# Kernel tuning notes

Measured on AMD Instinct MI355X. Metric: run time of the kernel, lower is better.

Reference implementation:

```python
import jax, jax.numpy as jnp
import numpy as np

N = 100_000   # nodes
E = 3_200_000 # edges (avg degree 32)
H = 128       # hidden units
G = 64        # graphs in batch
EPS = 1e-5    # BatchNorm eps


def setup_inputs() -> dict:
    key = jax.random.key(0)
    ks = jax.random.split(key, 32)
    s = 0.05
    inp = {
        "x": jax.random.normal(ks[0], (N, 1), dtype=jnp.float32),
        "edge_index": jax.random.randint(ks[1], (2, E), 0, N, dtype=jnp.int64 if jax.config.jax_enable_x64 else jnp.int32),
        "batch": jnp.sort(jax.random.randint(ks[2], (N,), 0, G, dtype=jnp.int64 if jax.config.jax_enable_x64 else jnp.int32)),
    }
    dims = [(1, H), (H, H), (H, H)]
    k = 3
    for li, (cin, cout) in enumerate(dims, start=1):
        inp[f"W_rel{li}"] = jax.random.normal(ks[k], (cout, cin), dtype=jnp.float32) * s; k += 1
        inp[f"b_rel{li}"] = jax.random.normal(ks[k], (cout,), dtype=jnp.float32) * s; k += 1
        inp[f"W_root{li}"] = jax.random.normal(ks[k], (cout, cin), dtype=jnp.float32) * s; k += 1
        inp[f"gamma{li}"] = jnp.ones((cout,), dtype=jnp.float32)
        inp[f"beta{li}"] = jnp.zeros((cout,), dtype=jnp.float32)
        inp[f"mean{li}"] = jax.random.normal(ks[k], (cout,), dtype=jnp.float32) * s; k += 1
        inp[f"var{li}"] = jax.random.uniform(ks[k], (cout,), dtype=jnp.float32, minval=0.5, maxval=1.5); k += 1
    inp["W_out"] = jax.random.normal(ks[k], (1, H), dtype=jnp.float32) * s; k += 1
    inp["b_out"] = jax.random.normal(ks[k], (1,), dtype=jnp.float32) * s
    return inp


def _graph_conv(x, src, dst, W_rel, b_rel, W_root):
    # PyG GraphConv (aggr='add'): out_i = W_rel @ sum_{j->i} x_j + b_rel + W_root @ x_i
    agg = jax.ops.segment_sum(x[src], dst, num_segments=N)  # [N, Cin]
    return agg @ W_rel.T + b_rel + x @ W_root.T


def _bn_eval(x, gamma, beta, mean, var):
    return (x - mean) * jax.lax.rsqrt(var + EPS) * gamma + beta


def reference(x, edge_index, batch,
              W_rel1, b_rel1, W_root1, gamma1, beta1, mean1, var1,
              W_rel2, b_rel2, W_root2, gamma2, beta2, mean2, var2,
              W_rel3, b_rel3, W_root3, gamma3, beta3, mean3, var3,
              W_out, b_out):
    src, dst = edge_index[0], edge_index[1]
    h = _graph_conv(x, src, dst, W_rel1, b_rel1, W_root1)
    h = jax.nn.relu(_bn_eval(h, gamma1, beta1, mean1, var1))  # dropout p=0 / eval -> identity
    h = _graph_conv(h, src, dst, W_rel2, b_rel2, W_root2)
    h = jax.nn.relu(_bn_eval(h, gamma2, beta2, mean2, var2))
    h = _graph_conv(h, src, dst, W_rel3, b_rel3, W_root3)
    h = _bn_eval(h, gamma3, beta3, mean3, var3)
    # global mean pool over graphs
    sums = jax.ops.segment_sum(h, batch, num_segments=G)                       # [G, H]
    cnts = jax.ops.segment_sum(jnp.ones((N, 1), h.dtype), batch, num_segments=G)
    pooled = sums / jnp.maximum(cnts, 1.0)
    return pooled @ W_out.T + b_out  # [G, 1]
```

## Files before the change

### kernel.cpp

```cpp
#include <hip/hip_runtime.h>

typedef unsigned int uint;
typedef unsigned short ushort;
typedef unsigned char uchar;

#define EPS 1e-5f
#define BSH 8
#define NBMAX 512
#define BCAP 10240
#define SCAT_E 8192

typedef __attribute__((ext_vector_type(8))) short short8;
typedef __attribute__((ext_vector_type(16))) float f32x16;
typedef __attribute__((ext_vector_type(2))) float float2v;
typedef __attribute__((ext_vector_type(2))) _Float16 half2v;
typedef __attribute__((ext_vector_type(8))) _Float16 f16x8;

static __device__ __forceinline__ ushort f2h(float f) {
    return __builtin_bit_cast(ushort, (_Float16)f);
}
static __device__ __forceinline__ half2v u2h(uint u) {
    return __builtin_bit_cast(half2v, u);
}

__global__ __launch_bounds__(256) void hist2d_kernel(const int* __restrict__ dst,
                                                     int* __restrict__ cnt2d, int E, int NB) {
    __shared__ int lh[NBMAX];
    const int tid = threadIdx.x;
    for (int t = tid; t < NB; t += 256) lh[t] = 0;
    __syncthreads();
    const int base = blockIdx.x * SCAT_E, end = min(base + SCAT_E, E);
    for (int i = base + tid; i < end; i += 256) atomicAdd(&lh[dst[i] >> BSH], 1);
    __syncthreads();
    int* row = cnt2d + (size_t)blockIdx.x * NB;
    for (int t = tid; t < NB; t += 256) row[t] = lh[t];
}

__global__ __launch_bounds__(256) void scan2d_kernel(int* __restrict__ cnt2d,
                                                     int* __restrict__ bcnt, int NB, int NBLK) {
    const int b = blockIdx.x * 4 + (threadIdx.x >> 6);
    if (b >= NB) return;
    const int lane = threadIdx.x & 63;
    int carry = 0;
    for (int c0 = 0; c0 < NBLK; c0 += 64) {
        int idx = c0 + lane;
        int v = (idx < NBLK) ? cnt2d[(size_t)idx * NB + b] : 0;
        int inc = v;
#pragma unroll
        for (int d = 1; d < 64; d <<= 1) { int u = __shfl_up(inc, d); if (lane >= d) inc += u; }
        if (idx < NBLK) cnt2d[(size_t)idx * NB + b] = inc - v + carry;
        carry += __shfl(inc, 63);
    }
    if (lane == 0) bcnt[b] = carry;
}

__global__ void scan_gcur_kernel(const int* __restrict__ bcnt, int* __restrict__ gcur, int nb) {
    __shared__ int wsum[4];
    const int t = threadIdx.x;
    int e[4], s = 0;
#pragma unroll
    for (int k = 0; k < 4; ++k) {
        int idx = t * 4 + k;
        e[k] = (idx < nb) ? bcnt[idx] : 0;
        s += e[k];
    }
    int lane = t & 63, w = t >> 6;
    int v = s;
#pragma unroll
    for (int d = 1; d < 64; d <<= 1) { int u = __shfl_up(v, d); if (lane >= d) v += u; }
    if (lane == 63) wsum[w] = v;
    __syncthreads();
    int off = 0;
    for (int k = 0; k < w; ++k) off += wsum[k];
    int run = off + v - s;
#pragma unroll
    for (int k = 0; k < 4; ++k) {
        int idx = t * 4 + k;
        if (idx < nb) gcur[idx] = run;
        run += e[k];
    }
    if (t == 0) gcur[nb] = wsum[0] + wsum[1] + wsum[2] + wsum[3];
}

__global__ __launch_bounds__(256) void bucket_scatter_kernel(const int* __restrict__ src,
                                                             const int* __restrict__ dst,
                                                             const int* __restrict__ gcur,
                                                             const int* __restrict__ cnt2d,
                                                             uint* __restrict__ stage,
                                                             int E, int NB) {
    __shared__ uint sedge[SCAT_E];
    __shared__ ushort sbkt[SCAT_E];
    __shared__ int lh[NBMAX];
    __shared__ int lofs[NBMAX + 1];
    __shared__ int lbase[NBMAX];
    __shared__ int wsum[4];
    const int tid = threadIdx.x;
    const int base = blockIdx.x * SCAT_E;
    const int len = min(base + SCAT_E, E) - base;
    const int* myrow = cnt2d + (size_t)blockIdx.x * NB;

    for (int t = tid; t < NB; t += 256) lh[t] = 0;
    __syncthreads();
    for (int i = tid; i < len; i += 256) atomicAdd(&lh[dst[base + i] >> BSH], 1);
    __syncthreads();
    const int i0 = tid * 2, i1 = tid * 2 + 1;
    int e0 = (i0 < NB) ? lh[i0] : 0;
    int e1 = (i1 < NB) ? lh[i1] : 0;
    int s = e0 + e1;
    int lane = tid & 63, w = tid >> 6;
    int v = s;
#pragma unroll
    for (int d = 1; d < 64; d <<= 1) { int u = __shfl_up(v, d); if (lane >= d) v += u; }
    if (lane == 63) wsum[w] = v;
    __syncthreads();
    int off = 0;
    for (int k = 0; k < w; ++k) off += wsum[k];
    int run = off + v - s;
    if (i0 <= NB) lofs[i0] = run;
    if (i0 < NB) lbase[i0] = gcur[i0] + myrow[i0];
    run += e0;
    if (i1 <= NB) lofs[i1] = run;
    if (i1 < NB) lbase[i1] = gcur[i1] + myrow[i1];
    __syncthreads();
    for (int t = tid; t < NB; t += 256) lh[t] = 0;
    __syncthreads();
    for (int i = tid; i < len; i += 256) {
        int d = dst[base + i];
        int b = d >> BSH;
        int r = atomicAdd(&lh[b], 1);
        int pos = lofs[b] + r;
        sedge[pos] = (uint)src[base + i] | ((uint)(d & 255) << 17);
        sbkt[pos] = (ushort)b;
    }
    __syncthreads();
    for (int i = tid; i < len; i += 256) {
        int b = sbkt[i];
        stage[lbase[b] + (i - lofs[b])] = sedge[i];
    }
}

__global__ __launch_bounds__(256) void bucket_final_kernel(const uint* __restrict__ stage,
                                                           const int* __restrict__ gcur,
                                                           int* __restrict__ rowptr,
                                                           int* __restrict__ eidx, int n) {
    __shared__ uint sbuf[BCAP];
    __shared__ int cnt[256];
    __shared__ int wsum[4];
    const int b = blockIdx.x, tid = threadIdx.x;
    const int r0 = gcur[b];
    const int r1 = gcur[b + 1];
    const int len = r1 - r0;
    const bool inl = (len <= BCAP);
    cnt[tid] = 0;
    if (inl) for (int i = tid; i < len; i += 256) sbuf[i] = stage[r0 + i];
    __syncthreads();
    for (int i = tid; i < len; i += 256) {
        uint v = inl ? sbuf[i] : stage[r0 + i];
        atomicAdd(&cnt[v >> 17], 1);
    }
    __syncthreads();
    int orig = cnt[tid], v = orig;
    int lane = tid & 63, w = tid >> 6;
#pragma unroll
    for (int d2 = 1; d2 < 64; d2 <<= 1) { int u = __shfl_up(v, d2); if (lane >= d2) v += u; }
    if (lane == 63) wsum[w] = v;
    __syncthreads();
    int off = 0;
    for (int k = 0; k < w; ++k) off += wsum[k];
    const int excl = r0 + off + v - orig;
    const int d = (b << BSH) + tid;
    if (d <= n) rowptr[d] = excl;
    __syncthreads();
    cnt[tid] = excl;
    __syncthreads();
    for (int i = tid; i < len; i += 256) {
        uint pv = inl ? sbuf[i] : stage[r0 + i];
        int slot = atomicAdd(&cnt[pv >> 17], 1);
        eidx[slot] = (int)(pv & 0x1FFFFu);
    }
}

__global__ __launch_bounds__(256) void layer1_fused_kernel(
    const float* __restrict__ x, const int* __restrict__ rowptr, const int* __restrict__ eidx,
    const float* __restrict__ Wrel, const float* __restrict__ brel,
    const float* __restrict__ Wroot, const float* __restrict__ gamma,
    const float* __restrict__ beta, const float* __restrict__ mean,
    const float* __restrict__ var, ushort* __restrict__ h1, uchar* __restrict__ h8, int n) {
    __shared__ float A[128], B[128], C[128];
    const int tid = threadIdx.x;
    if (tid < 128) {
        float sc = gamma[tid] * rsqrtf(var[tid] + EPS);
        A[tid] = Wrel[tid] * sc;
        B[tid] = Wroot[tid] * sc;
        C[tid] = beta[tid] + (brel[tid] - mean[tid]) * sc;
    }
    __syncthreads();
    const int g16 = tid >> 4;
    const int l16 = tid & 15;
    const int node = blockIdx.x * 16 + g16;
    if (node >= n) return;
    const int e0 = rowptr[node], e1 = rowptr[node + 1];
    float acc = 0.f;
    for (int e = e0 + l16; e < e1; e += 16) acc += x[eidx[e]];
#pragma unroll
    for (int d = 1; d < 16; d <<= 1) acc += __shfl_xor(acc, d);
    const float xi = x[node];
    float vv[8];
    uint4 o;
    ushort* op = (ushort*)&o;
#pragma unroll
    for (int j = 0; j < 8; ++j) {
        int c = l16 * 8 + j;
        vv[j] = fmaxf(acc * A[c] + xi * B[c] + C[c], 0.f);
        op[j] = f2h(vv[j]);
    }
    *((uint4*)(h1 + (size_t)node * 128) + l16) = o;
    uint p0 = 0, p1 = 0;
    p0 = __builtin_amdgcn_cvt_pk_fp8_f32(vv[0], vv[1], 0, 0);
    p0 = __builtin_amdgcn_cvt_pk_fp8_f32(vv[2], vv[3], p0, 1);
    p1 = __builtin_amdgcn_cvt_pk_fp8_f32(vv[4], vv[5], 0, 0);
    p1 = __builtin_amdgcn_cvt_pk_fp8_f32(vv[6], vv[7], p1, 1);
    uint2 o8; o8.x = p0; o8.y = p1;
    ((uint2*)(h8 + (size_t)node * 128))[l16] = o8;
}

__global__ __launch_bounds__(256) void gather_fp8_kernel(const uchar* __restrict__ h8,
                                                         const int* __restrict__ rowptr,
                                                         const int* __restrict__ eidx,
                                                         ushort* __restrict__ agg, int n) {
    const int node = blockIdx.x * 4 + (threadIdx.x >> 6);
    if (node >= n) return;
    const int lane = threadIdx.x & 63;
    const int g = lane >> 4;
    const int c8 = lane & 15;
    const uint2* hq = (const uint2*)h8;
    const int e0 = rowptr[node];
    const int len = rowptr[node + 1] - e0;

    float2v a0 = {0.f, 0.f}, a1 = {0.f, 0.f}, a2 = {0.f, 0.f}, a3 = {0.f, 0.f};

#define ACC8(u)                                                        \
    do {                                                               \
        a0 += __builtin_amdgcn_cvt_pk_f32_fp8((int)(u).x, 0);          \
        a1 += __builtin_amdgcn_cvt_pk_f32_fp8((int)(u).x, 1);          \
        a2 += __builtin_amdgcn_cvt_pk_f32_fp8((int)(u).y, 0);          \
        a3 += __builtin_amdgcn_cvt_pk_f32_fp8((int)(u).y, 1);          \
    } while (0)

    for (int base = 0; base < len; base += 64) {
        const int cnt = min(len - base, 64);
        int msrc = (lane < cnt) ? eidx[e0 + base + lane] : 0;
        const int kfull = cnt >> 2;
        int k = 0;
        for (; k + 8 <= kfull; k += 8) {
            uint2 u[8];
#pragma unroll
            for (int s = 0; s < 8; ++s) {
                int src = __shfl(msrc, (k + s) * 4 + g);
                u[s] = hq[(size_t)src * 16 + c8];
            }
#pragma unroll
            for (int s = 0; s < 8; ++s) ACC8(u[s]);
        }
        for (; k < kfull; ++k) {
            int src = __shfl(msrc, k * 4 + g);
            uint2 u = hq[(size_t)src * 16 + c8];
            ACC8(u);
        }
        const int rem = cnt & 3;
        if (rem) {
            int idx = (kfull << 2) + g;
            int src = __shfl(msrc, idx);
            if (g < rem) {
                uint2 u = hq[(size_t)src * 16 + c8];
                ACC8(u);
            }
        }
    }
#undef ACC8

#pragma unroll
    for (int d = 16; d <= 32; d <<= 1) {
        a0[0] += __shfl_xor(a0[0], d); a0[1] += __shfl_xor(a0[1], d);
        a1[0] += __shfl_xor(a1[0], d); a1[1] += __shfl_xor(a1[1], d);
        a2[0] += __shfl_xor(a2[0], d); a2[1] += __shfl_xor(a2[1], d);
        a3[0] += __shfl_xor(a3[0], d); a3[1] += __shfl_xor(a3[1], d);
    }
    if (g == 0) {
        uint4 o;
        ushort* op = (ushort*)&o;
        op[0] = f2h(a0[0]); op[1] = f2h(a0[1]);
        op[2] = f2h(a1[0]); op[3] = f2h(a1[1]);
        op[4] = f2h(a2[0]); op[5] = f2h(a2[1]);
        op[6] = f2h(a3[0]); op[7] = f2h(a3[1]);
        ((uint4*)agg)[(size_t)node * 16 + c8] = o;
    }
}

__global__ void wf_prep_kernel(const float* __restrict__ W0, const float* __restrict__ W1,
                               const float* __restrict__ W2, const float* __restrict__ W3,
                               ushort* __restrict__ WF2, ushort* __restrict__ WF3) {
    int i = blockIdx.x * 256 + threadIdx.x;
    const float* Ws[4] = {W0, W1, W2, W3};
    int mat = i >> 14;
    int m = i & 16383;
    int j = m & 7, lane = (m >> 3) & 63, ct = (m >> 9) & 3, kt = (m >> 11) & 7;
    int row = ct * 32 + (lane & 31);
    int col = kt * 16 + ((lane >> 5) * 8) + j;
    float v = Ws[mat][row * 128 + col];
    ushort* dstp = (mat < 2) ? WF2 : WF3;
    dstp[(mat & 1) * 16384 + m] = f2h(v);
}

template <int RELU, int WRITE8>
__global__ __launch_bounds__(256) void conv_mfma_kernel(
    const short* __restrict__ agg, const short* __restrict__ hin,
    const short* __restrict__ WF,
    const float* __restrict__ brel, const float* __restrict__ gamma,
    const float* __restrict__ beta, const float* __restrict__ mean,
    const float* __restrict__ var,
    ushort* __restrict__ hout, uchar* __restrict__ h8out, int n) {
    const int lane = threadIdx.x & 63;
    const int wt = blockIdx.x * 4 + (threadIdx.x >> 6);
    const int node0 = wt * 32;
    if (node0 >= n) return;
    const int rowA = node0 + (lane & 31);
    const int arow = (rowA < n) ? rowA : (n - 1);
    const int koff = (lane >> 5) * 8;

    f32x16 acc[4];
#pragma unroll
    for (int c = 0; c < 4; ++c) acc[c] = (f32x16)(0.0f);

#pragma unroll
    for (int half = 0; half < 2; ++half) {
        const short* A = (half ? hin : agg) + (size_t)arow * 128 + koff;
        const short* B0 = WF + half * 16384 + lane * 8;
#pragma unroll
        for (int kt = 0; kt < 8; ++kt) {
            f16x8 a = __builtin_bit_cast(f16x8, *(const short8*)(A + kt * 16));
            const short* Bp = B0 + kt * 2048;
#pragma unroll
            for (int ct = 0; ct < 4; ++ct) {
                f16x8 b = __builtin_bit_cast(f16x8, *(const short8*)(Bp + ct * 512));
                acc[ct] = __builtin_amdgcn_mfma_f32_32x32x16_f16(a, b, acc[ct], 0, 0, 0);
            }
        }
    }

#pragma unroll
    for (int ct = 0; ct < 4; ++ct) {
        int c = ct * 32 + (lane & 31);
        float s = gamma[c] * rsqrtf(var[c] + EPS);
        float t = beta[c] - mean[c] * s + brel[c] * s;
#pragma unroll
        for (int r = 0; r < 16; ++r) {
            int row = (r & 3) + 8 * (r >> 2) + 4 * (lane >> 5);
            int node = node0 + row;
            if (node < n) {
                float v = acc[ct][r] * s + t;
                if (RELU) v = fmaxf(v, 0.f);
                hout[(size_t)node * 128 + c] = f2h(v);
                if (WRITE8) {
                    uint p = __builtin_amdgcn_cvt_pk_fp8_f32(v, v, 0, 0);
                    h8out[(size_t)node * 128 + c] = (uchar)p;
                }
            }
        }
    }
}

__global__ __launch_bounds__(256) void pool_kernel(const ushort* __restrict__ h,
                                                   const int* __restrict__ batch,
                                                   const float* __restrict__ Wout,
                                                   float* __restrict__ gscal,
                                                   int* __restrict__ gcnt, int n) {
    const int wv = blockIdx.x * 4 + (threadIdx.x >> 6);
    const int lane = threadIdx.x & 63;
    const int base = wv * 64;
    if (base >= n) return;
    const int end = min(base + 64, n);
    const uint* hu = (const uint*)h;
    const float w0 = Wout[lane * 2], w1 = Wout[lane * 2 + 1];
    float s = 0.f;
    int cur = batch[base], cl = 0;

    auto accum = [&](uint u) {
        half2v hv = u2h(u);
        s += (float)hv[0] * w0 + (float)hv[1] * w1;
        cl++;
    };
    auto flush = [&](int g) {
        float r = s;
#pragma unroll
        for (int d = 1; d < 64; d <<= 1) r += __shfl_xor(r, d);
        if (lane == 0) { atomicAdd(&gscal[g], r); atomicAdd(&gcnt[g], cl); }
        s = 0.f; cl = 0;
    };

    int i = base;
    for (; i + 4 <= end; i += 4) {
        int b3 = batch[i + 3];
        uint u0 = hu[(size_t)i * 64 + lane];
        uint u1 = hu[(size_t)(i + 1) * 64 + lane];
        uint u2 = hu[(size_t)(i + 2) * 64 + lane];
        uint u3 = hu[(size_t)(i + 3) * 64 + lane];
        if (b3 == cur) {
            accum(u0); accum(u1); accum(u2); accum(u3);
        } else {
            int bb[4] = {batch[i], batch[i + 1], batch[i + 2], b3};
            uint uu[4] = {u0, u1, u2, u3};
            for (int k = 0; k < 4; ++k) {
                if (bb[k] != cur) { flush(cur); cur = bb[k]; }
                accum(uu[k]);
            }
        }
    }
    for (; i < end; ++i) {
        int g = batch[i];
        if (g != cur) { flush(cur); cur = g; }
        accum(hu[(size_t)i * 64 + lane]);
    }
    flush(cur);
}

__global__ void out_kernel(const float* __restrict__ gscal, const int* __restrict__ gcnt,
                           const float* __restrict__ bout, float* __restrict__ out, int G) {
    int g = threadIdx.x;
    if (g < G) out[g] = gscal[g] / fmaxf((float)gcnt[g], 1.0f) + bout[0];
}

extern "C" void kernel_launch(void* const* d_in, const int* in_sizes, int n_in,
                              void* d_out, int out_size, void* d_ws, size_t ws_size,
                              hipStream_t stream) {
    const int N = in_sizes[0];
    const int E = in_sizes[1] / 2;
    const int G = 64;

    const float* x     = (const float*)d_in[0];
    const int*   ei    = (const int*)d_in[1];
    const int*   batch = (const int*)d_in[2];
    const int*   src   = ei;
    const int*   dst   = ei + E;

    const float* Wrel1 = (const float*)d_in[3];
    const float* brel1 = (const float*)d_in[4];
    const float* Wroot1= (const float*)d_in[5];
    const float* g1    = (const float*)d_in[6];
    const float* be1   = (const float*)d_in[7];
    const float* m1    = (const float*)d_in[8];
    const float* v1    = (const float*)d_in[9];
    const float* Wrel2 = (const float*)d_in[10];
    const float* brel2 = (const float*)d_in[11];
    const float* Wroot2= (const float*)d_in[12];
    const float* g2    = (const float*)d_in[13];
    const float* be2   = (const float*)d_in[14];
    const float* m2    = (const float*)d_in[15];
    const float* v2    = (const float*)d_in[16];
    const float* Wrel3 = (const float*)d_in[17];
    const float* brel3 = (const float*)d_in[18];
    const float* Wroot3= (const float*)d_in[19];
    const float* g3    = (const float*)d_in[20];
    const float* be3   = (const float*)d_in[21];
    const float* m3    = (const float*)d_in[22];
    const float* v3    = (const float*)d_in[23];
    const float* Wout  = (const float*)d_in[24];
    const float* bout  = (const float*)d_in[25];

    float* out = (float*)d_out;

    const int NB   = (N >> BSH) + 1;
    const int NBLK = (E + SCAT_E - 1) / SCAT_E;

    char* w = (char*)d_ws;
    auto alloc = [&](size_t bytes) { char* p = w; w += (bytes + 511) & ~(size_t)511; return p; };
    int*    rowptr = (int*)alloc((size_t)(N + 1) * 4);
    int*    bcnt   = (int*)alloc(NBMAX * 4);
    int*    gcur   = (int*)alloc((NBMAX + 1) * 4);
    int*    cnt2d  = (int*)alloc((size_t)NBLK * NB * 4);
    uint*   stage  = (uint*)alloc((size_t)E * 4);
    int*    eidx   = (int*)alloc((size_t)E * 4);
    ushort* hA     = (ushort*)alloc((size_t)N * 128 * 2);
    ushort* hB     = (ushort*)alloc((size_t)N * 128 * 2);
    ushort* aggb   = (ushort*)alloc((size_t)N * 128 * 2);
    uchar*  h8     = (uchar*)alloc((size_t)N * 128);
    ushort* WF2    = (ushort*)alloc(32768 * 2);
    ushort* WF3    = (ushort*)alloc(32768 * 2);
    float*  gscal  = (float*)alloc((size_t)G * 4);
    int*    gcnt   = (int*)alloc((size_t)G * 4);

    hipMemsetAsync(gscal, 0, (size_t)G * 4, stream);
    hipMemsetAsync(gcnt, 0, (size_t)G * 4, stream);

    hist2d_kernel<<<NBLK, 256, 0, stream>>>(dst, cnt2d, E, NB);
    scan2d_kernel<<<(NB + 3) / 4, 256, 0, stream>>>(cnt2d, bcnt, NB, NBLK);
    scan_gcur_kernel<<<1, 256, 0, stream>>>(bcnt, gcur, NB);
    bucket_scatter_kernel<<<NBLK, 256, 0, stream>>>(src, dst, gcur, cnt2d, stage, E, NB);
    bucket_final_kernel<<<NB, 256, 0, stream>>>(stage, gcur, rowptr, eidx, N);

    wf_prep_kernel<<<256, 256, 0, stream>>>(Wrel2, Wroot2, Wrel3, Wroot3, WF2, WF3);

    layer1_fused_kernel<<<(N + 15) / 16, 256, 0, stream>>>(x, rowptr, eidx, Wrel1, brel1,
                                                           Wroot1, g1, be1, m1, v1, hA, h8, N);

    const int nwt     = (N + 31) / 32;
    const int convBlk = (nwt + 3) / 4;
    const int gBlk    = (N + 3) / 4;

    gather_fp8_kernel<<<gBlk, 256, 0, stream>>>(h8, rowptr, eidx, aggb, N);
    conv_mfma_kernel<1, 1><<<convBlk, 256, 0, stream>>>((const short*)aggb, (const short*)hA,
                                                        (const short*)WF2, brel2, g2, be2, m2, v2,
                                                        hB, h8, N);

    gather_fp8_kernel<<<gBlk, 256, 0, stream>>>(h8, rowptr, eidx, aggb, N);
    conv_mfma_kernel<0, 0><<<convBlk, 256, 0, stream>>>((const short*)aggb, (const short*)hB,
                                                        (const short*)WF3, brel3, g3, be3, m3, v3,
                                                        hA, (uchar*)nullptr, N);

    pool_kernel<<<(N + 255) / 256, 256, 0, stream>>>(hA, batch, Wout, gscal, gcnt, N);
    out_kernel<<<1, 64, 0, stream>>>(gscal, gcnt, bout, out, G);
}
```

Measured before the change: 300.6 us.

## Fuse fp8 gather, MFMA conv and mean-pool into a single per-layer kernel

Merges the neighbor gather into the MFMA GraphConv kernel. Each block gathers 32 nodes' aggregated features into swizzled LDS and then multiplies them directly, so the fp16 agg buffer is never written to or read from global memory. The last layer also folds the output projection and per-graph pooling into the epilogue using LDS atomics, which removes the hA write and the separate pool kernel. Ping-pong fp8 buffers replace the single h8 buffer so a layer's write does not race its own gather reads. The trade-offs are fewer blocks with serialized per-wave gathers (8 nodes per wave), one output column tile per wave, and LDS atomics in the pool epilogue.

```diff
diff --git a/kernel.cpp b/kernel.cpp
--- a/kernel.cpp
+++ b/kernel.cpp
@@ -224,79 +224,6 @@
     ((uint2*)(h8 + (size_t)node * 128))[l16] = o8;
 }
 
-__global__ __launch_bounds__(256) void gather_fp8_kernel(const uchar* __restrict__ h8,
-                                                         const int* __restrict__ rowptr,
-                                                         const int* __restrict__ eidx,
-                                                         ushort* __restrict__ agg, int n) {
-    const int node = blockIdx.x * 4 + (threadIdx.x >> 6);
-    if (node >= n) return;
-    const int lane = threadIdx.x & 63;
-    const int g = lane >> 4;
-    const int c8 = lane & 15;
-    const uint2* hq = (const uint2*)h8;
-    const int e0 = rowptr[node];
-    const int len = rowptr[node + 1] - e0;
-
-    float2v a0 = {0.f, 0.f}, a1 = {0.f, 0.f}, a2 = {0.f, 0.f}, a3 = {0.f, 0.f};
-
-#define ACC8(u)                                                        \
-    do {                                                               \
-        a0 += __builtin_amdgcn_cvt_pk_f32_fp8((int)(u).x, 0);          \
-        a1 += __builtin_amdgcn_cvt_pk_f32_fp8((int)(u).x, 1);          \
-        a2 += __builtin_amdgcn_cvt_pk_f32_fp8((int)(u).y, 0);          \
-        a3 += __builtin_amdgcn_cvt_pk_f32_fp8((int)(u).y, 1);          \
-    } while (0)
-
-    for (int base = 0; base < len; base += 64) {
-        const int cnt = min(len - base, 64);
-        int msrc = (lane < cnt) ? eidx[e0 + base + lane] : 0;
-        const int kfull = cnt >> 2;
-        int k = 0;
-        for (; k + 8 <= kfull; k += 8) {
-            uint2 u[8];
-#pragma unroll
-            for (int s = 0; s < 8; ++s) {
-                int src = __shfl(msrc, (k + s) * 4 + g);
-                u[s] = hq[(size_t)src * 16 + c8];
-            }
-#pragma unroll
-            for (int s = 0; s < 8; ++s) ACC8(u[s]);
-        }
-        for (; k < kfull; ++k) {
-            int src = __shfl(msrc, k * 4 + g);
-            uint2 u = hq[(size_t)src * 16 + c8];
-            ACC8(u);
-        }
-        const int rem = cnt & 3;
-        if (rem) {
-            int idx = (kfull << 2) + g;
-            int src = __shfl(msrc, idx);
-            if (g < rem) {
-                uint2 u = hq[(size_t)src * 16 + c8];
-                ACC8(u);
-            }
-        }
-    }
-#undef ACC8
-
-#pragma unroll
-    for (int d = 16; d <= 32; d <<= 1) {
-        a0[0] += __shfl_xor(a0[0], d); a0[1] += __shfl_xor(a0[1], d);
-        a1[0] += __shfl_xor(a1[0], d); a1[1] += __shfl_xor(a1[1], d);
-        a2[0] += __shfl_xor(a2[0], d); a2[1] += __shfl_xor(a2[1], d);
-        a3[0] += __shfl_xor(a3[0], d); a3[1] += __shfl_xor(a3[1], d);
-    }
-    if (g == 0) {
-        uint4 o;
-        ushort* op = (ushort*)&o;
-        op[0] = f2h(a0[0]); op[1] = f2h(a0[1]);
-        op[2] = f2h(a1[0]); op[3] = f2h(a1[1]);
-        op[4] = f2h(a2[0]); op[5] = f2h(a2[1]);
-        op[6] = f2h(a3[0]); op[7] = f2h(a3[1]);
-        ((uint4*)agg)[(size_t)node * 16 + c8] = o;
-    }
-}
-
 __global__ void wf_prep_kernel(const float* __restrict__ W0, const float* __restrict__ W1,
                                const float* __restrict__ W2, const float* __restrict__ W3,
                                ushort* __restrict__ WF2, ushort* __restrict__ WF3) {
@@ -312,53 +239,125 @@
     dstp[(mat & 1) * 16384 + m] = f2h(v);
 }
 
-template <int RELU, int WRITE8>
-__global__ __launch_bounds__(256) void conv_mfma_kernel(
-    const short* __restrict__ agg, const short* __restrict__ hin,
-    const short* __restrict__ WF,
+template <int RELU, int WRITE8, int POOL>
+__global__ __launch_bounds__(256) void gc_kernel(
+    const uchar* __restrict__ h8in, const int* __restrict__ rowptr, const int* __restrict__ eidx,
+    const short* __restrict__ hin, const short* __restrict__ WF,
     const float* __restrict__ brel, const float* __restrict__ gamma,
     const float* __restrict__ beta, const float* __restrict__ mean,
     const float* __restrict__ var,
-    ushort* __restrict__ hout, uchar* __restrict__ h8out, int n) {
-    const int lane = threadIdx.x & 63;
-    const int wt = blockIdx.x * 4 + (threadIdx.x >> 6);
-    const int node0 = wt * 32;
-    if (node0 >= n) return;
-    const int rowA = node0 + (lane & 31);
-    const int arow = (rowA < n) ? rowA : (n - 1);
+    ushort* __restrict__ hout, uchar* __restrict__ h8out,
+    const int* __restrict__ batch, const float* __restrict__ Wout,
+    float* __restrict__ gscal, int* __restrict__ gcnt, int n) {
+    __shared__ uint4 aggL[32][16];
+    __shared__ float pg[64];
+    __shared__ int pc[64];
+    const int tid = threadIdx.x;
+    if (POOL && tid < 64) { pg[tid] = 0.f; pc[tid] = 0; }
+    const int w = tid >> 6, lane = tid & 63, g = lane >> 4, c8 = lane & 15;
+    const uint2* hq = (const uint2*)h8in;
+    const int T = blockIdx.x * 32;
+
+    for (int nd = 0; nd < 8; ++nd) {
+        const int rr = w * 8 + nd;
+        const int node = T + rr;
+        if (node >= n) break;
+        const int e0 = rowptr[node];
+        const int len = rowptr[node + 1] - e0;
+        float2v a0 = {0.f, 0.f}, a1 = {0.f, 0.f}, a2 = {0.f, 0.f}, a3 = {0.f, 0.f};
+
+#define ACC8(u)                                                        \
+    do {                                                               \
+        a0 += __builtin_amdgcn_cvt_pk_f32_fp8((int)(u).x, 0);          \
+        a1 += __builtin_amdgcn_cvt_pk_f32_fp8((int)(u).x, 1);          \
+        a2 += __builtin_amdgcn_cvt_pk_f32_fp8((int)(u).y, 0);          \
+        a3 += __builtin_amdgcn_cvt_pk_f32_fp8((int)(u).y, 1);          \
+    } while (0)
+
+        for (int base = 0; base < len; base += 64) {
+            const int cnt = min(len - base, 64);
+            int msrc = (lane < cnt) ? eidx[e0 + base + lane] : 0;
+            const int kfull = cnt >> 2;
+            int k = 0;
+            for (; k + 8 <= kfull; k += 8) {
+                uint2 u[8];
+#pragma unroll
+                for (int s = 0; s < 8; ++s) {
+                    int src = __shfl(msrc, (k + s) * 4 + g);
+                    u[s] = hq[(size_t)src * 16 + c8];
+                }
+#pragma unroll
+                for (int s = 0; s < 8; ++s) ACC8(u[s]);
+            }
+            for (; k < kfull; ++k) {
+                int src = __shfl(msrc, k * 4 + g);
+                uint2 u = hq[(size_t)src * 16 + c8];
+                ACC8(u);
+            }
+            const int rem = cnt & 3;
+            if (rem) {
+                int idx = (kfull << 2) + g;
+                int src = __shfl(msrc, idx);
+                if (g < rem) {
+                    uint2 u = hq[(size_t)src * 16 + c8];
+                    ACC8(u);
+                }
+            }
+        }
+#undef ACC8
+#pragma unroll
+        for (int d = 16; d <= 32; d <<= 1) {
+            a0[0] += __shfl_xor(a0[0], d); a0[1] += __shfl_xor(a0[1], d);
+            a1[0] += __shfl_xor(a1[0], d); a1[1] += __shfl_xor(a1[1], d);
+            a2[0] += __shfl_xor(a2[0], d); a2[1] += __shfl_xor(a2[1], d);
+            a3[0] += __shfl_xor(a3[0], d); a3[1] += __shfl_xor(a3[1], d);
+        }
+        if (g == 0) {
+            uint4 o;
+            ushort* op = (ushort*)&o;
+            op[0] = f2h(a0[0]); op[1] = f2h(a0[1]);
+            op[2] = f2h(a1[0]); op[3] = f2h(a1[1]);
+            op[4] = f2h(a2[0]); op[5] = f2h(a2[1]);
+            op[6] = f2h(a3[0]); op[7] = f2h(a3[1]);
+            aggL[rr][c8 ^ (rr & 7)] = o;
+        }
+    }
+    __syncthreads();
+
+    const int ct = w;
+    const int r32 = lane & 31;
     const int koff = (lane >> 5) * 8;
-
-    f32x16 acc[4];
-#pragma unroll
-    for (int c = 0; c < 4; ++c) acc[c] = (f32x16)(0.0f);
-
-#pragma unroll
-    for (int half = 0; half < 2; ++half) {
-        const short* A = (half ? hin : agg) + (size_t)arow * 128 + koff;
-        const short* B0 = WF + half * 16384 + lane * 8;
+    const int arow = (T + r32 < n) ? (T + r32) : (n - 1);
+    f32x16 acc = (f32x16)(0.0f);
+    {
+        const short* B0 = WF + ct * 512 + lane * 8;
 #pragma unroll
         for (int kt = 0; kt < 8; ++kt) {
-            f16x8 a = __builtin_bit_cast(f16x8, *(const short8*)(A + kt * 16));
-            const short* Bp = B0 + kt * 2048;
-#pragma unroll
-            for (int ct = 0; ct < 4; ++ct) {
-                f16x8 b = __builtin_bit_cast(f16x8, *(const short8*)(Bp + ct * 512));
-                acc[ct] = __builtin_amdgcn_mfma_f32_32x32x16_f16(a, b, acc[ct], 0, 0, 0);
-            }
-        }
-    }
-
-#pragma unroll
-    for (int ct = 0; ct < 4; ++ct) {
-        int c = ct * 32 + (lane & 31);
-        float s = gamma[c] * rsqrtf(var[c] + EPS);
-        float t = beta[c] - mean[c] * s + brel[c] * s;
+            int ch = 2 * kt + (koff >> 3);
+            uint4 av = aggL[r32][ch ^ (r32 & 7)];
+            f16x8 a = __builtin_bit_cast(f16x8, av);
+            f16x8 b = __builtin_bit_cast(f16x8, *(const short8*)(B0 + kt * 2048));
+            acc = __builtin_amdgcn_mfma_f32_32x32x16_f16(a, b, acc, 0, 0, 0);
+        }
+        const short* A1 = hin + (size_t)arow * 128 + koff;
+        const short* B1 = WF + 16384 + ct * 512 + lane * 8;
+#pragma unroll
+        for (int kt = 0; kt < 8; ++kt) {
+            f16x8 a = __builtin_bit_cast(f16x8, *(const short8*)(A1 + kt * 16));
+            f16x8 b = __builtin_bit_cast(f16x8, *(const short8*)(B1 + kt * 2048));
+            acc = __builtin_amdgcn_mfma_f32_32x32x16_f16(a, b, acc, 0, 0, 0);
+        }
+    }
+    const int c = ct * 32 + r32;
+    float s = gamma[c] * rsqrtf(var[c] + EPS);
+    float t = beta[c] - mean[c] * s + brel[c] * s;
+    if (!POOL) {
 #pragma unroll
         for (int r = 0; r < 16; ++r) {
             int row = (r & 3) + 8 * (r >> 2) + 4 * (lane >> 5);
-            int node = node0 + row;
+            int node = T + row;
             if (node < n) {
-                float v = acc[ct][r] * s + t;
+                float v = acc[r] * s + t;
                 if (RELU) v = fmaxf(v, 0.f);
                 hout[(size_t)node * 128 + c] = f2h(v);
                 if (WRITE8) {
@@ -367,61 +366,27 @@
                 }
             }
         }
-    }
-}
-
-__global__ __launch_bounds__(256) void pool_kernel(const ushort* __restrict__ h,
-                                                   const int* __restrict__ batch,
-                                                   const float* __restrict__ Wout,
-                                                   float* __restrict__ gscal,
-                                                   int* __restrict__ gcnt, int n) {
-    const int wv = blockIdx.x * 4 + (threadIdx.x >> 6);
-    const int lane = threadIdx.x & 63;
-    const int base = wv * 64;
-    if (base >= n) return;
-    const int end = min(base + 64, n);
-    const uint* hu = (const uint*)h;
-    const float w0 = Wout[lane * 2], w1 = Wout[lane * 2 + 1];
-    float s = 0.f;
-    int cur = batch[base], cl = 0;
-
-    auto accum = [&](uint u) {
-        half2v hv = u2h(u);
-        s += (float)hv[0] * w0 + (float)hv[1] * w1;
-        cl++;
-    };
-    auto flush = [&](int g) {
-        float r = s;
-#pragma unroll
-        for (int d = 1; d < 64; d <<= 1) r += __shfl_xor(r, d);
-        if (lane == 0) { atomicAdd(&gscal[g], r); atomicAdd(&gcnt[g], cl); }
-        s = 0.f; cl = 0;
-    };
-
-    int i = base;
-    for (; i + 4 <= end; i += 4) {
-        int b3 = batch[i + 3];
-        uint u0 = hu[(size_t)i * 64 + lane];
-        uint u1 = hu[(size_t)(i + 1) * 64 + lane];
-        uint u2 = hu[(size_t)(i + 2) * 64 + lane];
-        uint u3 = hu[(size_t)(i + 3) * 64 + lane];
-        if (b3 == cur) {
-            accum(u0); accum(u1); accum(u2); accum(u3);
-        } else {
-            int bb[4] = {batch[i], batch[i + 1], batch[i + 2], b3};
-            uint uu[4] = {u0, u1, u2, u3};
-            for (int k = 0; k < 4; ++k) {
-                if (bb[k] != cur) { flush(cur); cur = bb[k]; }
-                accum(uu[k]);
+    } else {
+        const float wq = Wout[c];
+#pragma unroll
+        for (int r = 0; r < 16; ++r) {
+            int row = (r & 3) + 8 * (r >> 2) + 4 * (lane >> 5);
+            int node = T + row;
+            float v = (node < n) ? (acc[r] * s + t) * wq : 0.f;
+#pragma unroll
+            for (int d = 1; d < 32; d <<= 1) v += __shfl_xor(v, d);
+            if (r32 == 0 && node < n) {
+                int gg = batch[node];
+                atomicAdd(&pg[gg], v);
+                if (ct == 0) atomicAdd(&pc[gg], 1);
             }
         }
-    }
-    for (; i < end; ++i) {
-        int g = batch[i];
-        if (g != cur) { flush(cur); cur = g; }
-        accum(hu[(size_t)i * 64 + lane]);
-    }
-    flush(cur);
+        __syncthreads();
+        if (tid < 64 && pc[tid]) {
+            atomicAdd(&gcnt[tid], pc[tid]);
+            atomicAdd(&gscal[tid], pg[tid]);
+        }
+    }
 }
 
 __global__ void out_kernel(const float* __restrict__ gscal, const int* __restrict__ gcnt,
@@ -482,8 +447,8 @@
     int*    eidx   = (int*)alloc((size_t)E * 4);
     ushort* hA     = (ushort*)alloc((size_t)N * 128 * 2);
     ushort* hB     = (ushort*)alloc((size_t)N * 128 * 2);
-    ushort* aggb   = (ushort*)alloc((size_t)N * 128 * 2);
-    uchar*  h8     = (uchar*)alloc((size_t)N * 128);
+    uchar*  h8a    = (uchar*)alloc((size_t)N * 128);
+    uchar*  h8b    = (uchar*)alloc((size_t)N * 128);
     ushort* WF2    = (ushort*)alloc(32768 * 2);
     ushort* WF3    = (ushort*)alloc(32768 * 2);
     float*  gscal  = (float*)alloc((size_t)G * 4);
@@ -501,22 +466,17 @@
     wf_prep_kernel<<<256, 256, 0, stream>>>(Wrel2, Wroot2, Wrel3, Wroot3, WF2, WF3);
 
     layer1_fused_kernel<<<(N + 15) / 16, 256, 0, stream>>>(x, rowptr, eidx, Wrel1, brel1,
-                                                           Wroot1, g1, be1, m1, v1, hA, h8, N);
-
-    const int nwt     = (N + 31) / 32;
-    const int convBlk = (nwt + 3) / 4;
-    const int gBlk    = (N + 3) / 4;
-
-    gather_fp8_kernel<<<gBlk, 256, 0, stream>>>(h8, rowptr, eidx, aggb, N);
-    conv_mfma_kernel<1, 1><<<convBlk, 256, 0, stream>>>((const short*)aggb, (const short*)hA,
-                                                        (const short*)WF2, brel2, g2, be2, m2, v2,
-                                                        hB, h8, N);
-
-    gather_fp8_kernel<<<gBlk, 256, 0, stream>>>(h8, rowptr, eidx, aggb, N);
-    conv_mfma_kernel<0, 0><<<convBlk, 256, 0, stream>>>((const short*)aggb, (const short*)hB,
-                                                        (const short*)WF3, brel3, g3, be3, m3, v3,
-                                                        hA, (uchar*)nullptr, N);
-
-    pool_kernel<<<(N + 255) / 256, 256, 0, stream>>>(hA, batch, Wout, gscal, gcnt, N);
+                                                           Wroot1, g1, be1, m1, v1, hA, h8a, N);
+
+    const int gcBlk = (N + 31) / 32;
+
+    gc_kernel<1, 1, 0><<<gcBlk, 256, 0, stream>>>(h8a, rowptr, eidx, (const short*)hA,
+                                                  (const short*)WF2, brel2, g2, be2, m2, v2,
+                                                  hB, h8b, nullptr, nullptr, nullptr, nullptr, N);
+
+    gc_kernel<0, 0, 1><<<gcBlk, 256, 0, stream>>>(h8b, rowptr, eidx, (const short*)hB,
+                                                  (const short*)WF3, brel3, g3, be3, m3, v3,
+                                                  nullptr, nullptr, batch, Wout, gscal, gcnt, N);
+
     out_kernel<<<1, 64, 0, stream>>>(gscal, gcnt, bout, out, G);
 }
```

Result: slower. 359.8 us (+19.7%).
